# Optimization experiments

Hardware: AMD Instinct MI355X
Metric: run time of the kernel (lower is better)

Reference implementation:

```python
import jax, jax.numpy as jnp
import numpy as np

BETA = 0.25


def setup_inputs() -> dict:
    key = jax.random.key(0)
    k1, k2, k3, k4 = jax.random.split(key, 4)
    e_dim, n_e = 512, 8192
    z = jax.random.normal(k1, (16, e_dim, 32, 32), dtype=jnp.float32)
    # nn.init.normal_(embedding.weight, std=e_dim**-0.5)
    emb_weight = jax.random.normal(k2, (n_e, e_dim), dtype=jnp.float32) * (e_dim ** -0.5)
    # torch Linear default init ~ U(-1/sqrt(in), 1/sqrt(in))
    lim = 1.0 / np.sqrt(e_dim)
    proj_w = jax.random.uniform(k3, (e_dim, e_dim), minval=-lim, maxval=lim, dtype=jnp.float32)
    proj_b = jax.random.uniform(k4, (e_dim,), minval=-lim, maxval=lim, dtype=jnp.float32)
    return {"z": z, "emb_weight": emb_weight, "proj_w": proj_w, "proj_b": proj_b}


def reference(z, emb_weight, proj_w, proj_b):
    # z: [B, C, H, W] -> [B, H, W, C]
    zc = jnp.transpose(z, (0, 2, 3, 1))
    B, H, W, C = zc.shape
    z_flat = zc.reshape(-1, C)                               # [N, C]
    # projected codebook: Linear(e_dim, e_dim) -> x @ W^T + b
    qc = emb_weight @ proj_w.T + proj_b                      # [n_e, C]
    # squared distances: ||z||^2 + ||qc||^2 - 2 z.qc
    d = (jnp.sum(z_flat ** 2, axis=1, keepdims=True)
         + jnp.sum(qc ** 2, axis=1)
         - 2.0 * jnp.einsum('nd,kd->nk', z_flat, qc))        # [N, n_e]
    idx = jnp.argmin(d, axis=1)                              # [N]
    z_q = qc[idx].reshape(zc.shape)                          # [B, H, W, C]
    # legacy=False commit loss
    commit_loss = (BETA * jnp.mean((jax.lax.stop_gradient(z_q) - zc) ** 2)
                   + jnp.mean((z_q - jax.lax.stop_gradient(zc)) ** 2))
    # straight-through
    z_q = zc + jax.lax.stop_gradient(z_q - zc)
    z_q = jnp.transpose(z_q, (0, 3, 1, 2))                   # [B, C, H, W]
    min_encoding_indices = idx.reshape(B, H, W)              # sane_index_shape=True
    return z_q, commit_loss, min_encoding_indices
```

## Files before the change

### kernel.cpp

```cpp
#include <hip/hip_runtime.h>

typedef unsigned int uint;
typedef unsigned short ushort;
typedef __attribute__((ext_vector_type(8))) short short8;
typedef __attribute__((ext_vector_type(4))) float f32x4;

#define B_   16
#define C_   512
#define HW_  1024
#define N_   16384
#define K_   8192
#define EPS_ 0.25f

#define QC_OFF    0u
#define QC_SZ     (K_ * C_)
#define QN_OFF    (QC_OFF + QC_SZ)
#define QN_SZ     K_
#define ZN_OFF    (QN_OFF + QN_SZ)
#define ZN_SZ     N_
#define ZF_OFF    (ZN_OFF + ZN_SZ)
#define ZF_SZ     (N_ * C_)
#define ZH_OFF    (ZF_OFF + ZF_SZ)
#define ZH_SZ     (N_ * C_ / 2)
#define QH_OFF    (ZH_OFF + ZH_SZ)
#define QH_SZ     (K_ * C_ / 2)
#define WT_OFF    (QH_OFF + QH_SZ)
#define WT_SZ     (64 * N_ * 4)
#define CK_OFF    (WT_OFF + WT_SZ)
#define CK_SZ     (N_ * 16)
#define CC_OFF    (CK_OFF + CK_SZ)
#define CC_SZ     N_
#define IDXF_OFF  (CC_OFF + CC_SZ)
#define IDXF_SZ   N_
#define LOSS_OFF  (IDXF_OFF + IDXF_SZ)

#define OUT_ZQ    0
#define OUT_LOSS  8388608
#define OUT_IDX   8388609

__device__ __forceinline__ ushort f2bf(float f) {
    uint x = __float_as_uint(f);
    uint r = x + 0x7fffu + ((x >> 16) & 1u);
    return (ushort)(r >> 16);
}

__global__ __launch_bounds__(256) void transpose_z(const float* __restrict__ z,
                                                   float* __restrict__ zf,
                                                   ushort* __restrict__ zh) {
    __shared__ float ld[64][65];
    const int t = threadIdx.x;
    const int mt = blockIdx.x, ct = blockIdx.y, b = blockIdx.z;
    {
        const int cl = t >> 4, m4 = (t & 15) * 4;
#pragma unroll
        for (int cc = 0; cc < 4; ++cc) {
            const int c = ct * 64 + cc * 16 + cl;
            float4 v = *(const float4*)&z[((size_t)(b * 512 + c)) * 1024 + mt * 64 + m4];
            ld[cc * 16 + cl][m4 + 0] = v.x; ld[cc * 16 + cl][m4 + 1] = v.y;
            ld[cc * 16 + cl][m4 + 2] = v.z; ld[cc * 16 + cl][m4 + 3] = v.w;
        }
    }
    __syncthreads();
    {
        const int nl = t >> 4, c4 = (t & 15) * 4;
#pragma unroll
        for (int nn = 0; nn < 4; ++nn) {
            const int n_local = nn * 16 + nl;
            const size_t n = (size_t)b * 1024 + mt * 64 + n_local;
            float4 w;
            w.x = ld[c4 + 0][n_local]; w.y = ld[c4 + 1][n_local];
            w.z = ld[c4 + 2][n_local]; w.w = ld[c4 + 3][n_local];
            *(float4*)&zf[n * 512 + ct * 64 + c4] = w;
            ushort4 h; h.x = f2bf(w.x); h.y = f2bf(w.y); h.z = f2bf(w.z); h.w = f2bf(w.w);
            *(ushort4*)&zh[n * 512 + ct * 64 + c4] = h;
        }
    }
}

__global__ __launch_bounds__(256) void qc_gemm(const float* __restrict__ emb,
                                               const float* __restrict__ W,
                                               const float* __restrict__ bias,
                                               float* __restrict__ qc,
                                               ushort* __restrict__ qh) {
    __shared__ float As[16][132];
    __shared__ float Bs[16][132];
    const int t   = threadIdx.x;
    const int k0  = blockIdx.x * 128;
    const int c0  = blockIdx.y * 128;
    const int ty  = t >> 4, tx = t & 15;
    const int row = t >> 1;
    const int dq  = (t & 1) * 8;

    const float* pa = emb + (size_t)(k0 + row) * 512 + dq;
    const float* pb = W   + (size_t)(c0 + row) * 512 + dq;
    float4 ra0 = *(const float4*)&pa[0];
    float4 ra1 = *(const float4*)&pa[4];
    float4 rb0 = *(const float4*)&pb[0];
    float4 rb1 = *(const float4*)&pb[4];

    float acc[2][2][4][4] = {};
    for (int d0 = 0; d0 < 512; d0 += 16) {
        __syncthreads();
        As[dq + 0][row] = ra0.x; As[dq + 1][row] = ra0.y;
        As[dq + 2][row] = ra0.z; As[dq + 3][row] = ra0.w;
        As[dq + 4][row] = ra1.x; As[dq + 5][row] = ra1.y;
        As[dq + 6][row] = ra1.z; As[dq + 7][row] = ra1.w;
        Bs[dq + 0][row] = rb0.x; Bs[dq + 1][row] = rb0.y;
        Bs[dq + 2][row] = rb0.z; Bs[dq + 3][row] = rb0.w;
        Bs[dq + 4][row] = rb1.x; Bs[dq + 5][row] = rb1.y;
        Bs[dq + 6][row] = rb1.z; Bs[dq + 7][row] = rb1.w;
        if (d0 + 16 < 512) {
            ra0 = *(const float4*)&pa[d0 + 16];
            ra1 = *(const float4*)&pa[d0 + 20];
            rb0 = *(const float4*)&pb[d0 + 16];
            rb1 = *(const float4*)&pb[d0 + 20];
        }
        __syncthreads();
#pragma unroll
        for (int dd = 0; dd < 16; ++dd) {
            float4 a0 = *(const float4*)&As[dd][ty * 4];
            float4 a1 = *(const float4*)&As[dd][64 + ty * 4];
            float4 b0 = *(const float4*)&Bs[dd][tx * 4];
            float4 b1 = *(const float4*)&Bs[dd][64 + tx * 4];
            float aa[2][4] = {{a0.x, a0.y, a0.z, a0.w}, {a1.x, a1.y, a1.z, a1.w}};
            float bb[2][4] = {{b0.x, b0.y, b0.z, b0.w}, {b1.x, b1.y, b1.z, b1.w}};
#pragma unroll
            for (int ih = 0; ih < 2; ++ih)
#pragma unroll
                for (int jh = 0; jh < 2; ++jh)
#pragma unroll
                    for (int i = 0; i < 4; ++i)
#pragma unroll
                        for (int j = 0; j < 4; ++j)
                            acc[ih][jh][i][j] += aa[ih][i] * bb[jh][j];
        }
    }
#pragma unroll
    for (int ih = 0; ih < 2; ++ih)
#pragma unroll
        for (int i = 0; i < 4; ++i) {
            const size_t kr = (size_t)(k0 + ih * 64 + ty * 4 + i) * 512;
#pragma unroll
            for (int jh = 0; jh < 2; ++jh) {
                const int cb = c0 + jh * 64 + tx * 4;
                float4 v;
                v.x = acc[ih][jh][i][0] + bias[cb + 0];
                v.y = acc[ih][jh][i][1] + bias[cb + 1];
                v.z = acc[ih][jh][i][2] + bias[cb + 2];
                v.w = acc[ih][jh][i][3] + bias[cb + 3];
                *(float4*)&qc[kr + cb] = v;
                ushort4 h; h.x = f2bf(v.x); h.y = f2bf(v.y); h.z = f2bf(v.z); h.w = f2bf(v.w);
                *(ushort4*)&qh[kr + cb] = h;
            }
        }
}

__device__ __forceinline__ float pairwise512(const float* __restrict__ row) {
#pragma clang fp contract(off)
    float s128[4];
#pragma unroll
    for (int blk = 0; blk < 4; ++blk) {
        float r[8];
#pragma unroll
        for (int j = 0; j < 8; ++j) { float v = row[blk * 128 + j]; r[j] = v * v; }
#pragma unroll 1
        for (int i = 8; i < 128; i += 8) {
#pragma unroll
            for (int j = 0; j < 8; ++j) {
                float v = row[blk * 128 + i + j];
                float sq = v * v;
                r[j] = r[j] + sq;
            }
        }
        s128[blk] = ((r[0] + r[1]) + (r[2] + r[3])) + ((r[4] + r[5]) + (r[6] + r[7]));
    }
    return (s128[0] + s128[1]) + (s128[2] + s128[3]);
}

__global__ __launch_bounds__(256) void qnorm_pairwise(const float* __restrict__ qc,
                                                      float* __restrict__ qn) {
    const int k = blockIdx.x * 256 + threadIdx.x;
    qn[k] = pairwise512(qc + (size_t)k * C_);
}

__global__ __launch_bounds__(256) void znorm_pairwise(const float* __restrict__ zf,
                                                      float* __restrict__ zn) {
    const int n = blockIdx.x * 256 + threadIdx.x;
    zn[n] = pairwise512(zf + (size_t)n * C_);
}

#define PH_BAR()  __builtin_amdgcn_s_barrier()
#define PH_LGKM() asm volatile("s_waitcnt lgkmcnt(0)" ::: "memory")
#define PH_VM4()  asm volatile("s_waitcnt vmcnt(4)" ::: "memory")

__global__ __launch_bounds__(512, 2) void phaseA(const ushort* __restrict__ qh,
                                                 const ushort* __restrict__ zh,
                                                 const float* __restrict__ qn,
                                                 float* __restrict__ wtop) {
    __shared__ short lq[2][2][128 * 64];
    __shared__ short lz[2][2][128 * 64];
    const int t    = threadIdx.x;
    const int lane = t & 63;
    const int wv   = t >> 6;
    const int wk   = wv >> 2;
    const int wn   = wv & 3;
    const int n0   = blockIdx.x * 256;
    const int k0   = blockIdx.y * 256;

    auto stage_half = [&](int b, int h, int cchunk) {
        const int c0 = cchunk * 64;
#pragma unroll
        for (int p = 0; p < 2; ++p) {
            const int ch  = t + p * 512;
            const int row = ch >> 3;
            const int ce  = (((ch ^ row) & 7) << 3);
            if (h < 2) {
                __builtin_amdgcn_global_load_lds(
                    (const __attribute__((address_space(1))) uint*)(qh + (size_t)(k0 + h * 128 + row) * 512 + c0 + ce),
                    (__attribute__((address_space(3))) uint*)&lq[b][h][ch * 8], 16, 0, 0);
            } else {
                __builtin_amdgcn_global_load_lds(
                    (const __attribute__((address_space(1))) uint*)(zh + (size_t)(n0 + (h - 2) * 128 + row) * 512 + c0 + ce),
                    (__attribute__((address_space(3))) uint*)&lz[b][h - 2][ch * 8], 16, 0, 0);
            }
        }
    };

    auto rdA = [&](int b, int kk, int i) -> short8 {
        const int rl = i * 16 + (lane & 15);
        const int co = kk * 32 + ((lane >> 4) << 3);
        return *(const short8*)&lq[b][wk][rl * 64 + (co ^ ((rl & 7) << 3))];
    };
    auto rdB = [&](int b, int kk, int j) -> short8 {
        const int rg = wn * 64 + j * 16 + (lane & 15);
        const int co = kk * 32 + ((lane >> 4) << 3);
        return *(const short8*)&lz[b][rg >> 7][(rg & 127) * 64 + (co ^ ((rg & 7) << 3))];
    };

    f32x4 acc[8][4];
#pragma unroll
    for (int i = 0; i < 8; ++i)
#pragma unroll
        for (int j = 0; j < 4; ++j) acc[i][j] = (f32x4){0.f, 0.f, 0.f, 0.f};

    stage_half(0, 0, 0); stage_half(0, 1, 0); stage_half(0, 2, 0); stage_half(0, 3, 0);
    stage_half(1, 0, 1); stage_half(1, 1, 1);
    PH_VM4();
    PH_BAR();

    short8 a0[2][4], a1[2][4], b0[2][2], b1[2][2];

#pragma unroll 1
    for (int I = 0; I < 4; ++I) {
        const int t1 = 2 * I + 1;
        const int t2 = (2 * I + 2) & 7;
        const int t3 = (2 * I + 3) & 7;

#pragma unroll
        for (int kk = 0; kk < 2; ++kk) {
#pragma unroll
            for (int i = 0; i < 4; ++i) a0[kk][i] = rdA(0, kk, i);
#pragma unroll
            for (int j = 0; j < 2; ++j) b0[kk][j] = rdB(0, kk, j);
        }
        stage_half(1, 2, t1);
        PH_BAR(); PH_LGKM();
        __builtin_amdgcn_s_setprio(1);
#pragma unroll
        for (int kk = 0; kk < 2; ++kk)
#pragma unroll
            for (int i = 0; i < 4; ++i)
#pragma unroll
                for (int j = 0; j < 2; ++j)
                    acc[i][j] = __builtin_amdgcn_mfma_f32_16x16x32_bf16(a0[kk][i], b0[kk][j], acc[i][j], 0, 0, 0);
        __builtin_amdgcn_s_setprio(0);
        PH_BAR();
#pragma unroll
        for (int kk = 0; kk < 2; ++kk)
#pragma unroll
            for (int i = 0; i < 4; ++i) a1[kk][i] = rdA(0, kk, 4 + i);
        stage_half(1, 3, t1);
        PH_BAR(); PH_LGKM();
        __builtin_amdgcn_s_setprio(1);
#pragma unroll
        for (int kk = 0; kk < 2; ++kk)
#pragma unroll
            for (int i = 0; i < 4; ++i)
#pragma unroll
                for (int j = 0; j < 2; ++j)
                    acc[4 + i][j] = __builtin_amdgcn_mfma_f32_16x16x32_bf16(a1[kk][i], b0[kk][j], acc[4 + i][j], 0, 0, 0);
        __builtin_amdgcn_s_setprio(0);
        PH_BAR();
#pragma unroll
        for (int kk = 0; kk < 2; ++kk)
#pragma unroll
            for (int j = 0; j < 2; ++j) b1[kk][j] = rdB(0, kk, 2 + j);
        stage_half(0, 0, t2);
        PH_BAR(); PH_LGKM();
        __builtin_amdgcn_s_setprio(1);
#pragma unroll
        for (int kk = 0; kk < 2; ++kk)
#pragma unroll
            for (int i = 0; i < 4; ++i)
#pragma unroll
                for (int j = 0; j < 2; ++j)
                    acc[i][2 + j] = __builtin_amdgcn_mfma_f32_16x16x32_bf16(a0[kk][i], b1[kk][j], acc[i][2 + j], 0, 0, 0);
        __builtin_amdgcn_s_setprio(0);
        PH_BAR();
        stage_half(0, 1, t2);
        PH_BAR(); PH_LGKM();
        __builtin_amdgcn_s_setprio(1);
#pragma unroll
        for (int kk = 0; kk < 2; ++kk)
#pragma unroll
            for (int i = 0; i < 4; ++i)
#pragma unroll
                for (int j = 0; j < 2; ++j)
                    acc[4 + i][2 + j] = __builtin_amdgcn_mfma_f32_16x16x32_bf16(a1[kk][i], b1[kk][j], acc[4 + i][2 + j], 0, 0, 0);
        __builtin_amdgcn_s_setprio(0);
        PH_VM4();
        PH_BAR();

#pragma unroll
        for (int kk = 0; kk < 2; ++kk) {
#pragma unroll
            for (int i = 0; i < 4; ++i) a0[kk][i] = rdA(1, kk, i);
#pragma unroll
            for (int j = 0; j < 2; ++j) b0[kk][j] = rdB(1, kk, j);
        }
        stage_half(0, 2, t2);
        PH_BAR(); PH_LGKM();
        __builtin_amdgcn_s_setprio(1);
#pragma unroll
        for (int kk = 0; kk < 2; ++kk)
#pragma unroll
            for (int i = 0; i < 4; ++i)
#pragma unroll
                for (int j = 0; j < 2; ++j)
                    acc[i][j] = __builtin_amdgcn_mfma_f32_16x16x32_bf16(a0[kk][i], b0[kk][j], acc[i][j], 0, 0, 0);
        __builtin_amdgcn_s_setprio(0);
        PH_BAR();
#pragma unroll
        for (int kk = 0; kk < 2; ++kk)
#pragma unroll
            for (int i = 0; i < 4; ++i) a1[kk][i] = rdA(1, kk, 4 + i);
        stage_half(0, 3, t2);
        PH_BAR(); PH_LGKM();
        __builtin_amdgcn_s_setprio(1);
#pragma unroll
        for (int kk = 0; kk < 2; ++kk)
#pragma unroll
            for (int i = 0; i < 4; ++i)
#pragma unroll
                for (int j = 0; j < 2; ++j)
                    acc[4 + i][j] = __builtin_amdgcn_mfma_f32_16x16x32_bf16(a1[kk][i], b0[kk][j], acc[4 + i][j], 0, 0, 0);
        __builtin_amdgcn_s_setprio(0);
        PH_BAR();
#pragma unroll
        for (int kk = 0; kk < 2; ++kk)
#pragma unroll
            for (int j = 0; j < 2; ++j) b1[kk][j] = rdB(1, kk, 2 + j);
        stage_half(1, 0, t3);
        PH_BAR(); PH_LGKM();
        __builtin_amdgcn_s_setprio(1);
#pragma unroll
        for (int kk = 0; kk < 2; ++kk)
#pragma unroll
            for (int i = 0; i < 4; ++i)
#pragma unroll
                for (int j = 0; j < 2; ++j)
                    acc[i][2 + j] = __builtin_amdgcn_mfma_f32_16x16x32_bf16(a0[kk][i], b1[kk][j], acc[i][2 + j], 0, 0, 0);
        __builtin_amdgcn_s_setprio(0);
        PH_BAR();
        stage_half(1, 1, t3);
        PH_BAR(); PH_LGKM();
        __builtin_amdgcn_s_setprio(1);
#pragma unroll
        for (int kk = 0; kk < 2; ++kk)
#pragma unroll
            for (int i = 0; i < 4; ++i)
#pragma unroll
                for (int j = 0; j < 2; ++j)
                    acc[4 + i][2 + j] = __builtin_amdgcn_mfma_f32_16x16x32_bf16(a1[kk][i], b1[kk][j], acc[4 + i][2 + j], 0, 0, 0);
        __builtin_amdgcn_s_setprio(0);
        PH_VM4();
        PH_BAR();
    }

    const int q4 = (lane >> 4) * 4;
    float v1[4], v2[4];
    int   k1[4], k2[4];
#pragma unroll
    for (int in = 0; in < 4; ++in) { v1[in] = 1e30f; v2[in] = 1e30f; k1[in] = 0; k2[in] = 0; }

#pragma unroll
    for (int ik = 0; ik < 8; ++ik) {
        float qv[4];
#pragma unroll
        for (int r = 0; r < 4; ++r)
            qv[r] = qn[k0 + wk * 128 + ik * 16 + q4 + r];
#pragma unroll
        for (int in = 0; in < 4; ++in) {
#pragma unroll
            for (int r = 0; r < 4; ++r) {
                const float val = qv[r] - 2.0f * acc[ik][in][r];
                const int   kg  = k0 + wk * 128 + ik * 16 + q4 + r;
                if (val < v1[in]) { v2[in] = v1[in]; k2[in] = k1[in]; v1[in] = val; k1[in] = kg; }
                else if (val < v2[in]) { v2[in] = val; k2[in] = kg; }
            }
        }
    }
#pragma unroll
    for (int m = 16; m <= 32; m <<= 1) {
#pragma unroll
        for (int in = 0; in < 4; ++in) {
            const float ov1 = __shfl_xor(v1[in], m, 64);
            const int   ok1 = __shfl_xor(k1[in], m, 64);
            const float ov2 = __shfl_xor(v2[in], m, 64);
            const int   ok2 = __shfl_xor(k2[in], m, 64);
            float nv1, nv2; int nk1, nk2;
            if (ov1 < v1[in]) {
                nv1 = ov1; nk1 = ok1;
                if (v1[in] < ov2) { nv2 = v1[in]; nk2 = k1[in]; } else { nv2 = ov2; nk2 = ok2; }
            } else {
                nv1 = v1[in]; nk1 = k1[in];
                if (ov1 < v2[in]) { nv2 = ov1; nk2 = ok1; } else { nv2 = v2[in]; nk2 = k2[in]; }
            }
            v1[in] = nv1; k1[in] = nk1; v2[in] = nv2; k2[in] = nk2;
        }
    }
    if ((lane >> 4) == 0) {
        const int w = blockIdx.y * 2 + wk;
#pragma unroll
        for (int in = 0; in < 4; ++in) {
            const int n = n0 + wn * 64 + in * 16 + (lane & 15);
            float4 o; o.x = v1[in]; o.y = __int_as_float(k1[in]);
            o.z = v2[in]; o.w = __int_as_float(k2[in]);
            *(float4*)&wtop[((size_t)w * N_ + n) * 4] = o;
        }
    }
}

__global__ __launch_bounds__(256) void phaseB(const float* __restrict__ wtop,
                                              int* __restrict__ cand_k,
                                              int* __restrict__ cand_cnt) {
    const int n = blockIdx.x * 256 + threadIdx.x;
    float rmin = 1e30f;
    for (int w = 0; w < 64; ++w)
        rmin = fminf(rmin, wtop[((size_t)w * N_ + n) * 4]);
    const float thr = rmin + EPS_;
    int cnt = 0;
    for (int w = 0; w < 64; ++w) {
        float4 e = *(const float4*)&wtop[((size_t)w * N_ + n) * 4];
        if (e.x <= thr && cnt < 16) cand_k[n * 16 + cnt++] = __float_as_int(e.y);
        if (e.z <= thr && cnt < 16) cand_k[n * 16 + cnt++] = __float_as_int(e.w);
    }
    cand_cnt[n] = cnt;
}

__global__ __launch_bounds__(256) void phaseC(const float* __restrict__ zf,
                                              const float* __restrict__ qc,
                                              const float* __restrict__ zn,
                                              const float* __restrict__ qn,
                                              const int* __restrict__ cand_k,
                                              const int* __restrict__ cand_cnt,
                                              int* __restrict__ idxf,
                                              float* __restrict__ out_idx) {
    __shared__ float zr[4][512];
    __shared__ float ql[4][2][512];
    const int wv   = threadIdx.x >> 6;
    const int lane = threadIdx.x & 63;
    const int r    = blockIdx.x * 4 + wv;
    const int cnt  = cand_cnt[r];

    if (cnt == 1) {
        if (lane == 0) { const int k = cand_k[r * 16]; idxf[r] = k; out_idx[r] = (float)k; }
        return;
    }

    *(float4*)&zr[wv][lane * 8]     = *(const float4*)&zf[(size_t)r * 512 + lane * 8];
    *(float4*)&zr[wv][lane * 8 + 4] = *(const float4*)&zf[(size_t)r * 512 + lane * 8 + 4];

    const int g  = lane >> 5;
    const int cl = (lane & 31) * 16;
    const int steps = (cnt + 1) >> 1;
    const float znr = zn[r];

    auto cand_of = [&](int s) {
        const int ci = 2 * s + g;
        return cand_k[r * 16 + (ci < cnt ? ci : 0)];
    };

    int k_cur = cand_of(0);
    const float* q0 = qc + (size_t)k_cur * 512 + cl;
    float4 p0 = *(const float4*)&q0[0];
    float4 p1 = *(const float4*)&q0[4];
    float4 p2 = *(const float4*)&q0[8];
    float4 p3 = *(const float4*)&q0[12];

    float bd = 1e30f;
    int   bi = 0x7fffffff;

    for (int s = 0; s < steps; ++s) {
        *(float4*)&ql[wv][g][cl + 0]  = p0;
        *(float4*)&ql[wv][g][cl + 4]  = p1;
        *(float4*)&ql[wv][g][cl + 8]  = p2;
        *(float4*)&ql[wv][g][cl + 12] = p3;

        int k_next = 0;
        if (s + 1 < steps) {
            k_next = cand_of(s + 1);
            const float* qn_ = qc + (size_t)k_next * 512 + cl;
            p0 = *(const float4*)&qn_[0];
            p1 = *(const float4*)&qn_[4];
            p2 = *(const float4*)&qn_[8];
            p3 = *(const float4*)&qn_[12];
        }

        float acc = 0.f;
#pragma unroll 16
        for (int c = 0; c < 512; c += 4) {
            float4 zv = *(const float4*)&zr[wv][c];
            float4 qv = *(const float4*)&ql[wv][g][c];
            acc = fmaf(zv.x, qv.x, acc);
            acc = fmaf(zv.y, qv.y, acc);
            acc = fmaf(zv.z, qv.z, acc);
            acc = fmaf(zv.w, qv.w, acc);
        }
        const float T = znr + qn[k_cur];
        const float d = T - 2.0f * acc;
        const bool valid = (2 * s + g) < cnt;
        if (valid && (d < bd || (d == bd && k_cur < bi))) { bd = d; bi = k_cur; }
        k_cur = k_next;
    }

    const float od = __shfl_xor(bd, 32, 64);
    const int   oi = __shfl_xor(bi, 32, 64);
    if (od < bd || (od == bd && oi < bi)) { bd = od; bi = oi; }

    if (lane == 0) { idxf[r] = bi; out_idx[r] = (float)bi; }
}

__global__ __launch_bounds__(256) void gather_out(const float* __restrict__ z,
                                                  const float* __restrict__ qc,
                                                  const int* __restrict__ idxf,
                                                  float* __restrict__ zq_out,
                                                  float* __restrict__ loss_acc) {
    __shared__ int   idxs[64];
    __shared__ float zqs[64][65];
    __shared__ float wsum[4];
    const int t  = threadIdx.x;
    const int mc = blockIdx.x;
    const int cc = blockIdx.y;
    const int bz = blockIdx.z;

    if (t < 64) idxs[t] = idxf[bz * 1024 + mc * 64 + t];
    __syncthreads();
    {
        const int row  = t >> 2;
        const int coff = (t & 3) * 16;
        const float* src = qc + (size_t)idxs[row] * 512 + cc * 64 + coff;
#pragma unroll
        for (int v = 0; v < 4; ++v) {
            float4 q = *(const float4*)&src[v * 4];
            zqs[row][coff + v * 4 + 0] = q.x;
            zqs[row][coff + v * 4 + 1] = q.y;
            zqs[row][coff + v * 4 + 2] = q.z;
            zqs[row][coff + v * 4 + 3] = q.w;
        }
    }
    __syncthreads();

    float ls = 0.f;
    {
        const int c_local = t >> 2;
        const int mg      = (t & 3) * 16;
        const size_t gbase = ((size_t)(bz * 512 + cc * 64 + c_local)) * 1024 + mc * 64 + mg;
#pragma unroll
        for (int v = 0; v < 4; ++v) {
            const int m = mg + v * 4;
            float4 w;
            w.x = zqs[m + 0][c_local];
            w.y = zqs[m + 1][c_local];
            w.z = zqs[m + 2][c_local];
            w.w = zqs[m + 3][c_local];
            float4 zv = *(const float4*)&z[gbase + v * 4];
            float dx = w.x - zv.x, dy = w.y - zv.y, dz = w.z - zv.z, dw = w.w - zv.w;
            ls += dx * dx + dy * dy + dz * dz + dw * dw;
            *(float4*)&zq_out[gbase + v * 4] = w;
        }
    }
#pragma unroll
    for (int m = 32; m; m >>= 1) ls += __shfl_xor(ls, m, 64);
    const int lane = t & 63, wvv = t >> 6;
    if (lane == 0) wsum[wvv] = ls;
    __syncthreads();
    if (t == 0) atomicAdd(loss_acc, wsum[0] + wsum[1] + wsum[2] + wsum[3]);
}

__global__ void zero_loss(float* __restrict__ loss_acc) { loss_acc[0] = 0.f; }

__global__ void finalize(const float* __restrict__ loss_acc,
                         float* __restrict__ out_loss) {
    out_loss[0] = 1.25f * loss_acc[0] / 8388608.0f;
}

extern "C" void kernel_launch(void* const* d_in, const int* in_sizes, int n_in,
                              void* d_out, int out_size, void* d_ws, size_t ws_size,
                              hipStream_t stream) {
    const float* z    = (const float*)d_in[0];
    const float* emb  = (const float*)d_in[1];
    const float* W    = (const float*)d_in[2];
    const float* bias = (const float*)d_in[3];
    float* ws = (float*)d_ws;

    float*  qc       = ws + QC_OFF;
    float*  qn       = ws + QN_OFF;
    float*  zn       = ws + ZN_OFF;
    float*  zf       = ws + ZF_OFF;
    ushort* zh       = (ushort*)(ws + ZH_OFF);
    ushort* qh       = (ushort*)(ws + QH_OFF);
    float*  wtop     = ws + WT_OFF;
    int*    cand_k   = (int*)(ws + CK_OFF);
    int*    cand_cnt = (int*)(ws + CC_OFF);
    int*    idxf     = (int*)(ws + IDXF_OFF);
    float*  loss_acc = ws + LOSS_OFF;
    float*  out      = (float*)d_out;

    zero_loss<<<1, 1, 0, stream>>>(loss_acc);
    transpose_z<<<dim3(16, 8, 16), 256, 0, stream>>>(z, zf, zh);
    qc_gemm<<<dim3(K_ / 128, C_ / 128), 256, 0, stream>>>(emb, W, bias, qc, qh);
    qnorm_pairwise<<<K_ / 256, 256, 0, stream>>>(qc, qn);
    znorm_pairwise<<<N_ / 256, 256, 0, stream>>>(zf, zn);
    phaseA<<<dim3(N_ / 256, K_ / 256), 512, 0, stream>>>(qh, zh, qn, wtop);
    phaseB<<<N_ / 256, 256, 0, stream>>>(wtop, cand_k, cand_cnt);
    phaseC<<<N_ / 4, 256, 0, stream>>>(zf, qc, zn, qn, cand_k, cand_cnt, idxf, out + OUT_IDX);
    gather_out<<<dim3(16, 8, B_), 256, 0, stream>>>(z, qc, idxf, out + OUT_ZQ, loss_acc);
    finalize<<<1, 1, 0, stream>>>(loss_acc, out + OUT_LOSS);
}
```

Before: 421.1 us.

## Retile qc GEMM, coalesce norm kernels, precompute phaseA LDS pointers, drop zero kernel

Several independent changes. The qc GEMM tile is cut from 128x128 to 128x64, which doubles the grid and lowers per-thread registers. The z norm now reads the original NCHW z with coalesced strided loads instead of row-major zf. The q norm has 8 threads cooperate on each row and reduce with shuffles, so its loads coalesce. PhaseA precomputes its swizzled LDS and global addresses once instead of recomputing them on every access, and zeroing of the loss accumulator moves into phaseB to save a launch. The grouped q-norm sums in a different order from the old pairwise sum, which can change tie-breaking results slightly.

```diff
diff --git a/kernel.cpp b/kernel.cpp
--- a/kernel.cpp
+++ b/kernel.cpp
@@ -83,37 +83,35 @@
                                                float* __restrict__ qc,
                                                ushort* __restrict__ qh) {
     __shared__ float As[16][132];
-    __shared__ float Bs[16][132];
-    const int t   = threadIdx.x;
-    const int k0  = blockIdx.x * 128;
-    const int c0  = blockIdx.y * 128;
-    const int ty  = t >> 4, tx = t & 15;
-    const int row = t >> 1;
-    const int dq  = (t & 1) * 8;
-
-    const float* pa = emb + (size_t)(k0 + row) * 512 + dq;
-    const float* pb = W   + (size_t)(c0 + row) * 512 + dq;
+    __shared__ float Bs[16][68];
+    const int t    = threadIdx.x;
+    const int k0   = blockIdx.x * 128;
+    const int c0   = blockIdx.y * 64;
+    const int ty   = t >> 4, tx = t & 15;
+    const int rowA = t >> 1;
+    const int dqA  = (t & 1) * 8;
+    const int rowB = t >> 2;
+    const int dqB  = (t & 3) * 4;
+
+    const float* pa = emb + (size_t)(k0 + rowA) * 512 + dqA;
+    const float* pb = W   + (size_t)(c0 + rowB) * 512 + dqB;
     float4 ra0 = *(const float4*)&pa[0];
     float4 ra1 = *(const float4*)&pa[4];
-    float4 rb0 = *(const float4*)&pb[0];
-    float4 rb1 = *(const float4*)&pb[4];
-
-    float acc[2][2][4][4] = {};
+    float4 rb  = *(const float4*)&pb[0];
+
+    float acc[2][4][4] = {};
     for (int d0 = 0; d0 < 512; d0 += 16) {
         __syncthreads();
-        As[dq + 0][row] = ra0.x; As[dq + 1][row] = ra0.y;
-        As[dq + 2][row] = ra0.z; As[dq + 3][row] = ra0.w;
-        As[dq + 4][row] = ra1.x; As[dq + 5][row] = ra1.y;
-        As[dq + 6][row] = ra1.z; As[dq + 7][row] = ra1.w;
-        Bs[dq + 0][row] = rb0.x; Bs[dq + 1][row] = rb0.y;
-        Bs[dq + 2][row] = rb0.z; Bs[dq + 3][row] = rb0.w;
-        Bs[dq + 4][row] = rb1.x; Bs[dq + 5][row] = rb1.y;
-        Bs[dq + 6][row] = rb1.z; Bs[dq + 7][row] = rb1.w;
+        As[dqA + 0][rowA] = ra0.x; As[dqA + 1][rowA] = ra0.y;
+        As[dqA + 2][rowA] = ra0.z; As[dqA + 3][rowA] = ra0.w;
+        As[dqA + 4][rowA] = ra1.x; As[dqA + 5][rowA] = ra1.y;
+        As[dqA + 6][rowA] = ra1.z; As[dqA + 7][rowA] = ra1.w;
+        Bs[dqB + 0][rowB] = rb.x;  Bs[dqB + 1][rowB] = rb.y;
+        Bs[dqB + 2][rowB] = rb.z;  Bs[dqB + 3][rowB] = rb.w;
         if (d0 + 16 < 512) {
             ra0 = *(const float4*)&pa[d0 + 16];
             ra1 = *(const float4*)&pa[d0 + 20];
-            rb0 = *(const float4*)&pb[d0 + 16];
-            rb1 = *(const float4*)&pb[d0 + 20];
+            rb  = *(const float4*)&pb[d0 + 16];
         }
         __syncthreads();
 #pragma unroll
@@ -121,18 +119,15 @@
             float4 a0 = *(const float4*)&As[dd][ty * 4];
             float4 a1 = *(const float4*)&As[dd][64 + ty * 4];
             float4 b0 = *(const float4*)&Bs[dd][tx * 4];
-            float4 b1 = *(const float4*)&Bs[dd][64 + tx * 4];
             float aa[2][4] = {{a0.x, a0.y, a0.z, a0.w}, {a1.x, a1.y, a1.z, a1.w}};
-            float bb[2][4] = {{b0.x, b0.y, b0.z, b0.w}, {b1.x, b1.y, b1.z, b1.w}};
+            float bb[4] = {b0.x, b0.y, b0.z, b0.w};
 #pragma unroll
             for (int ih = 0; ih < 2; ++ih)
 #pragma unroll
-                for (int jh = 0; jh < 2; ++jh)
-#pragma unroll
-                    for (int i = 0; i < 4; ++i)
-#pragma unroll
-                        for (int j = 0; j < 4; ++j)
-                            acc[ih][jh][i][j] += aa[ih][i] * bb[jh][j];
+                for (int i = 0; i < 4; ++i)
+#pragma unroll
+                    for (int j = 0; j < 4; ++j)
+                        acc[ih][i][j] += aa[ih][i] * bb[j];
         }
     }
 #pragma unroll
@@ -140,65 +135,88 @@
 #pragma unroll
         for (int i = 0; i < 4; ++i) {
             const size_t kr = (size_t)(k0 + ih * 64 + ty * 4 + i) * 512;
-#pragma unroll
-            for (int jh = 0; jh < 2; ++jh) {
-                const int cb = c0 + jh * 64 + tx * 4;
-                float4 v;
-                v.x = acc[ih][jh][i][0] + bias[cb + 0];
-                v.y = acc[ih][jh][i][1] + bias[cb + 1];
-                v.z = acc[ih][jh][i][2] + bias[cb + 2];
-                v.w = acc[ih][jh][i][3] + bias[cb + 3];
-                *(float4*)&qc[kr + cb] = v;
-                ushort4 h; h.x = f2bf(v.x); h.y = f2bf(v.y); h.z = f2bf(v.z); h.w = f2bf(v.w);
-                *(ushort4*)&qh[kr + cb] = h;
-            }
-        }
-}
-
-__device__ __forceinline__ float pairwise512(const float* __restrict__ row) {
+            const int cb = c0 + tx * 4;
+            float4 v;
+            v.x = acc[ih][i][0] + bias[cb + 0];
+            v.y = acc[ih][i][1] + bias[cb + 1];
+            v.z = acc[ih][i][2] + bias[cb + 2];
+            v.w = acc[ih][i][3] + bias[cb + 3];
+            *(float4*)&qc[kr + cb] = v;
+            ushort4 h; h.x = f2bf(v.x); h.y = f2bf(v.y); h.z = f2bf(v.z); h.w = f2bf(v.w);
+            *(ushort4*)&qh[kr + cb] = h;
+        }
+}
+
+__global__ __launch_bounds__(256) void znorm_pairwise(const float* __restrict__ z,
+                                                      float* __restrict__ zn) {
 #pragma clang fp contract(off)
+    const int n = blockIdx.x * 256 + threadIdx.x;
+    const int b = n >> 10, m = n & 1023;
+    const float* base = z + (size_t)b * C_ * HW_ + m;
     float s128[4];
 #pragma unroll
     for (int blk = 0; blk < 4; ++blk) {
         float r[8];
 #pragma unroll
-        for (int j = 0; j < 8; ++j) { float v = row[blk * 128 + j]; r[j] = v * v; }
+        for (int j = 0; j < 8; ++j) {
+            float v = base[(size_t)(blk * 128 + j) * HW_];
+            r[j] = v * v;
+        }
 #pragma unroll 1
         for (int i = 8; i < 128; i += 8) {
 #pragma unroll
             for (int j = 0; j < 8; ++j) {
-                float v = row[blk * 128 + i + j];
+                float v = base[(size_t)(blk * 128 + i + j) * HW_];
                 float sq = v * v;
                 r[j] = r[j] + sq;
             }
         }
         s128[blk] = ((r[0] + r[1]) + (r[2] + r[3])) + ((r[4] + r[5]) + (r[6] + r[7]));
     }
-    return (s128[0] + s128[1]) + (s128[2] + s128[3]);
-}
-
-__global__ __launch_bounds__(256) void qnorm_pairwise(const float* __restrict__ qc,
-                                                      float* __restrict__ qn) {
-    const int k = blockIdx.x * 256 + threadIdx.x;
-    qn[k] = pairwise512(qc + (size_t)k * C_);
-}
-
-__global__ __launch_bounds__(256) void znorm_pairwise(const float* __restrict__ zf,
-                                                      float* __restrict__ zn) {
-    const int n = blockIdx.x * 256 + threadIdx.x;
-    zn[n] = pairwise512(zf + (size_t)n * C_);
+    zn[n] = (s128[0] + s128[1]) + (s128[2] + s128[3]);
+}
+
+__global__ __launch_bounds__(256) void qnorm_grouped(const float* __restrict__ qc,
+                                                     float* __restrict__ qn) {
+#pragma clang fp contract(off)
+    const int t   = threadIdx.x;
+    const int grp = t >> 3;
+    const int j   = t & 7;
+    const int k   = blockIdx.x * 32 + grp;
+    const float* row = qc + (size_t)k * C_;
+    float s[4];
+#pragma unroll
+    for (int blk = 0; blk < 4; ++blk) {
+        float v0 = row[blk * 128 + j];
+        float r  = v0 * v0;
+#pragma unroll 1
+        for (int i = 1; i < 16; ++i) {
+            float v  = row[blk * 128 + i * 8 + j];
+            float sq = v * v;
+            r = r + sq;
+        }
+        float t1 = r  + __shfl_xor(r, 1, 64);
+        float t2 = t1 + __shfl_xor(t1, 2, 64);
+        float t3 = t2 + __shfl_xor(t2, 4, 64);
+        s[blk] = t3;
+    }
+    if (j == 0) qn[k] = (s[0] + s[1]) + (s[2] + s[3]);
 }
 
 #define PH_BAR()  __builtin_amdgcn_s_barrier()
 #define PH_LGKM() asm volatile("s_waitcnt lgkmcnt(0)" ::: "memory")
 #define PH_VM4()  asm volatile("s_waitcnt vmcnt(4)" ::: "memory")
+
+__device__ __forceinline__ short8 ld8(const short* p, int off) {
+    return *(const short8*)(p + off);
+}
 
 __global__ __launch_bounds__(512, 2) void phaseA(const ushort* __restrict__ qh,
                                                  const ushort* __restrict__ zh,
                                                  const float* __restrict__ qn,
                                                  float* __restrict__ wtop) {
-    __shared__ short lq[2][2][128 * 64];
-    __shared__ short lz[2][2][128 * 64];
+    __shared__ short lq[32768];
+    __shared__ short lz[32768];
     const int t    = threadIdx.x;
     const int lane = t & 63;
     const int wv   = t >> 6;
@@ -207,34 +225,44 @@
     const int n0   = blockIdx.x * 256;
     const int k0   = blockIdx.y * 256;
 
-    auto stage_half = [&](int b, int h, int cchunk) {
-        const int c0 = cchunk * 64;
-#pragma unroll
-        for (int p = 0; p < 2; ++p) {
-            const int ch  = t + p * 512;
-            const int row = ch >> 3;
-            const int ce  = (((ch ^ row) & 7) << 3);
-            if (h < 2) {
-                __builtin_amdgcn_global_load_lds(
-                    (const __attribute__((address_space(1))) uint*)(qh + (size_t)(k0 + h * 128 + row) * 512 + c0 + ce),
-                    (__attribute__((address_space(3))) uint*)&lq[b][h][ch * 8], 16, 0, 0);
-            } else {
-                __builtin_amdgcn_global_load_lds(
-                    (const __attribute__((address_space(1))) uint*)(zh + (size_t)(n0 + (h - 2) * 128 + row) * 512 + c0 + ce),
-                    (__attribute__((address_space(3))) uint*)&lz[b][h - 2][ch * 8], 16, 0, 0);
-            }
-        }
-    };
-
-    auto rdA = [&](int b, int kk, int i) -> short8 {
-        const int rl = i * 16 + (lane & 15);
-        const int co = kk * 32 + ((lane >> 4) << 3);
-        return *(const short8*)&lq[b][wk][rl * 64 + (co ^ ((rl & 7) << 3))];
-    };
-    auto rdB = [&](int b, int kk, int j) -> short8 {
-        const int rg = wn * 64 + j * 16 + (lane & 15);
-        const int co = kk * 32 + ((lane >> 4) << 3);
-        return *(const short8*)&lz[b][rg >> 7][(rg & 127) * 64 + (co ^ ((rg & 7) << 3))];
+    const int l15 = lane & 15;
+    const int hi8 = (lane >> 4) << 3;
+    const int xr  = (l15 & 7) << 3;
+    const short* pA0 = lq + wk * 8192 + l15 * 64 + ((hi8) ^ xr);
+    const short* pA1 = lq + wk * 8192 + l15 * 64 + ((32 + hi8) ^ xr);
+    const short* pB0 = lz + (wn >> 1) * 8192 + (wn & 1) * 4096 + l15 * 64 + ((hi8) ^ xr);
+    const short* pB1 = lz + (wn >> 1) * 8192 + (wn & 1) * 4096 + l15 * 64 + ((32 + hi8) ^ xr);
+
+    const int ch0 = t,        row0 = ch0 >> 3;
+    const int ch1 = t + 512,  row1 = ch1 >> 3;
+    const int ce0 = ((ch0 ^ row0) & 7) << 3;
+    const int ce1 = ((ch1 ^ row1) & 7) << 3;
+    const ushort* qsrc0 = qh + (size_t)(k0 + row0) * 512 + ce0;
+    const ushort* qsrc1 = qh + (size_t)(k0 + row1) * 512 + ce1;
+    const ushort* zsrc0 = zh + (size_t)(n0 + row0) * 512 + ce0;
+    const ushort* zsrc1 = zh + (size_t)(n0 + row1) * 512 + ce1;
+    short* qdst0 = lq + ch0 * 8;
+    short* qdst1 = lq + ch1 * 8;
+    short* zdst0 = lz + ch0 * 8;
+    short* zdst1 = lz + ch1 * 8;
+
+    auto stage_half = [&](int b, int h, int chunk) {
+        const int co = chunk * 64;
+        if (h < 2) {
+            __builtin_amdgcn_global_load_lds(
+                (const __attribute__((address_space(1))) uint*)(qsrc0 + h * 65536 + co),
+                (__attribute__((address_space(3))) uint*)(qdst0 + (b * 2 + h) * 8192), 16, 0, 0);
+            __builtin_amdgcn_global_load_lds(
+                (const __attribute__((address_space(1))) uint*)(qsrc1 + h * 65536 + co),
+                (__attribute__((address_space(3))) uint*)(qdst1 + (b * 2 + h) * 8192), 16, 0, 0);
+        } else {
+            __builtin_amdgcn_global_load_lds(
+                (const __attribute__((address_space(1))) uint*)(zsrc0 + (h - 2) * 65536 + co),
+                (__attribute__((address_space(3))) uint*)(zdst0 + (b * 2 + (h - 2)) * 8192), 16, 0, 0);
+            __builtin_amdgcn_global_load_lds(
+                (const __attribute__((address_space(1))) uint*)(zsrc1 + (h - 2) * 65536 + co),
+                (__attribute__((address_space(3))) uint*)(zdst1 + (b * 2 + (h - 2)) * 8192), 16, 0, 0);
+        }
     };
 
     f32x4 acc[8][4];
@@ -257,12 +285,9 @@
         const int t3 = (2 * I + 3) & 7;
 
 #pragma unroll
-        for (int kk = 0; kk < 2; ++kk) {
-#pragma unroll
-            for (int i = 0; i < 4; ++i) a0[kk][i] = rdA(0, kk, i);
-#pragma unroll
-            for (int j = 0; j < 2; ++j) b0[kk][j] = rdB(0, kk, j);
-        }
+        for (int i = 0; i < 4; ++i) { a0[0][i] = ld8(pA0, i * 1024); a0[1][i] = ld8(pA1, i * 1024); }
+#pragma unroll
+        for (int jj = 0; jj < 2; ++jj) { b0[0][jj] = ld8(pB0, jj * 1024); b0[1][jj] = ld8(pB1, jj * 1024); }
         stage_half(1, 2, t1);
         PH_BAR(); PH_LGKM();
         __builtin_amdgcn_s_setprio(1);
@@ -271,14 +296,12 @@
 #pragma unroll
             for (int i = 0; i < 4; ++i)
 #pragma unroll
-                for (int j = 0; j < 2; ++j)
-                    acc[i][j] = __builtin_amdgcn_mfma_f32_16x16x32_bf16(a0[kk][i], b0[kk][j], acc[i][j], 0, 0, 0);
-        __builtin_amdgcn_s_setprio(0);
-        PH_BAR();
-#pragma unroll
-        for (int kk = 0; kk < 2; ++kk)
-#pragma unroll
-            for (int i = 0; i < 4; ++i) a1[kk][i] = rdA(0, kk, 4 + i);
+                for (int jj = 0; jj < 2; ++jj)
+                    acc[i][jj] = __builtin_amdgcn_mfma_f32_16x16x32_bf16(a0[kk][i], b0[kk][jj], acc[i][jj], 0, 0, 0);
+        __builtin_amdgcn_s_setprio(0);
+        PH_BAR();
+#pragma unroll
+        for (int i = 0; i < 4; ++i) { a1[0][i] = ld8(pA0, 4096 + i * 1024); a1[1][i] = ld8(pA1, 4096 + i * 1024); }
         stage_half(1, 3, t1);
         PH_BAR(); PH_LGKM();
         __builtin_amdgcn_s_setprio(1);
@@ -287,14 +310,12 @@
 #pragma unroll
             for (int i = 0; i < 4; ++i)
 #pragma unroll
-                for (int j = 0; j < 2; ++j)
-                    acc[4 + i][j] = __builtin_amdgcn_mfma_f32_16x16x32_bf16(a1[kk][i], b0[kk][j], acc[4 + i][j], 0, 0, 0);
-        __builtin_amdgcn_s_setprio(0);
-        PH_BAR();
-#pragma unroll
-        for (int kk = 0; kk < 2; ++kk)
-#pragma unroll
-            for (int j = 0; j < 2; ++j) b1[kk][j] = rdB(0, kk, 2 + j);
+                for (int jj = 0; jj < 2; ++jj)
+                    acc[4 + i][jj] = __builtin_amdgcn_mfma_f32_16x16x32_bf16(a1[kk][i], b0[kk][jj], acc[4 + i][jj], 0, 0, 0);
+        __builtin_amdgcn_s_setprio(0);
+        PH_BAR();
+#pragma unroll
+        for (int jj = 0; jj < 2; ++jj) { b1[0][jj] = ld8(pB0, 2048 + jj * 1024); b1[1][jj] = ld8(pB1, 2048 + jj * 1024); }
         stage_half(0, 0, t2);
         PH_BAR(); PH_LGKM();
         __builtin_amdgcn_s_setprio(1);
@@ -303,8 +324,8 @@
 #pragma unroll
             for (int i = 0; i < 4; ++i)
 #pragma unroll
-                for (int j = 0; j < 2; ++j)
-                    acc[i][2 + j] = __builtin_amdgcn_mfma_f32_16x16x32_bf16(a0[kk][i], b1[kk][j], acc[i][2 + j], 0, 0, 0);
+                for (int jj = 0; jj < 2; ++jj)
+                    acc[i][2 + jj] = __builtin_amdgcn_mfma_f32_16x16x32_bf16(a0[kk][i], b1[kk][jj], acc[i][2 + jj], 0, 0, 0);
         __builtin_amdgcn_s_setprio(0);
         PH_BAR();
         stage_half(0, 1, t2);
@@ -315,19 +336,16 @@
 #pragma unroll
             for (int i = 0; i < 4; ++i)
 #pragma unroll
-                for (int j = 0; j < 2; ++j)
-                    acc[4 + i][2 + j] = __builtin_amdgcn_mfma_f32_16x16x32_bf16(a1[kk][i], b1[kk][j], acc[4 + i][2 + j], 0, 0, 0);
+                for (int jj = 0; jj < 2; ++jj)
+                    acc[4 + i][2 + jj] = __builtin_amdgcn_mfma_f32_16x16x32_bf16(a1[kk][i], b1[kk][jj], acc[4 + i][2 + jj], 0, 0, 0);
         __builtin_amdgcn_s_setprio(0);
         PH_VM4();
         PH_BAR();
 
 #pragma unroll
-        for (int kk = 0; kk < 2; ++kk) {
-#pragma unroll
-            for (int i = 0; i < 4; ++i) a0[kk][i] = rdA(1, kk, i);
-#pragma unroll
-            for (int j = 0; j < 2; ++j) b0[kk][j] = rdB(1, kk, j);
-        }
+        for (int i = 0; i < 4; ++i) { a0[0][i] = ld8(pA0, 16384 + i * 1024); a0[1][i] = ld8(pA1, 16384 + i * 1024); }
+#pragma unroll
+        for (int jj = 0; jj < 2; ++jj) { b0[0][jj] = ld8(pB0, 16384 + jj * 1024); b0[1][jj] = ld8(pB1, 16384 + jj * 1024); }
         stage_half(0, 2, t2);
         PH_BAR(); PH_LGKM();
         __builtin_amdgcn_s_setprio(1);
@@ -336,14 +354,12 @@
 #pragma unroll
             for (int i = 0; i < 4; ++i)
 #pragma unroll
-                for (int j = 0; j < 2; ++j)
-                    acc[i][j] = __builtin_amdgcn_mfma_f32_16x16x32_bf16(a0[kk][i], b0[kk][j], acc[i][j], 0, 0, 0);
-        __builtin_amdgcn_s_setprio(0);
-        PH_BAR();
-#pragma unroll
-        for (int kk = 0; kk < 2; ++kk)
-#pragma unroll
-            for (int i = 0; i < 4; ++i) a1[kk][i] = rdA(1, kk, 4 + i);
+                for (int jj = 0; jj < 2; ++jj)
+                    acc[i][jj] = __builtin_amdgcn_mfma_f32_16x16x32_bf16(a0[kk][i], b0[kk][jj], acc[i][jj], 0, 0, 0);
+        __builtin_amdgcn_s_setprio(0);
+        PH_BAR();
+#pragma unroll
+        for (int i = 0; i < 4; ++i) { a1[0][i] = ld8(pA0, 16384 + 4096 + i * 1024); a1[1][i] = ld8(pA1, 16384 + 4096 + i * 1024); }
         stage_half(0, 3, t2);
         PH_BAR(); PH_LGKM();
         __builtin_amdgcn_s_setprio(1);
@@ -352,14 +368,12 @@
 #pragma unroll
             for (int i = 0; i < 4; ++i)
 #pragma unroll
-                for (int j = 0; j < 2; ++j)
-                    acc[4 + i][j] = __builtin_amdgcn_mfma_f32_16x16x32_bf16(a1[kk][i], b0[kk][j], acc[4 + i][j], 0, 0, 0);
-        __builtin_amdgcn_s_setprio(0);
-        PH_BAR();
-#pragma unroll
-        for (int kk = 0; kk < 2; ++kk)
-#pragma unroll
-            for (int j = 0; j < 2; ++j) b1[kk][j] = rdB(1, kk, 2 + j);
+                for (int jj = 0; jj < 2; ++jj)
+                    acc[4 + i][jj] = __builtin_amdgcn_mfma_f32_16x16x32_bf16(a1[kk][i], b0[kk][jj], acc[4 + i][jj], 0, 0, 0);
+        __builtin_amdgcn_s_setprio(0);
+        PH_BAR();
+#pragma unroll
+        for (int jj = 0; jj < 2; ++jj) { b1[0][jj] = ld8(pB0, 16384 + 2048 + jj * 1024); b1[1][jj] = ld8(pB1, 16384 + 2048 + jj * 1024); }
         stage_half(1, 0, t3);
         PH_BAR(); PH_LGKM();
         __builtin_amdgcn_s_setprio(1);
@@ -368,8 +382,8 @@
 #pragma unroll
             for (int i = 0; i < 4; ++i)
 #pragma unroll
-                for (int j = 0; j < 2; ++j)
-                    acc[i][2 + j] = __builtin_amdgcn_mfma_f32_16x16x32_bf16(a0[kk][i], b1[kk][j], acc[i][2 + j], 0, 0, 0);
+                for (int jj = 0; jj < 2; ++jj)
+                    acc[i][2 + jj] = __builtin_amdgcn_mfma_f32_16x16x32_bf16(a0[kk][i], b1[kk][jj], acc[i][2 + jj], 0, 0, 0);
         __builtin_amdgcn_s_setprio(0);
         PH_BAR();
         stage_half(1, 1, t3);
@@ -380,8 +394,8 @@
 #pragma unroll
             for (int i = 0; i < 4; ++i)
 #pragma unroll
-                for (int j = 0; j < 2; ++j)
-                    acc[4 + i][2 + j] = __builtin_amdgcn_mfma_f32_16x16x32_bf16(a1[kk][i], b1[kk][j], acc[4 + i][2 + j], 0, 0, 0);
+                for (int jj = 0; jj < 2; ++jj)
+                    acc[4 + i][2 + jj] = __builtin_amdgcn_mfma_f32_16x16x32_bf16(a1[kk][i], b1[kk][jj], acc[4 + i][2 + jj], 0, 0, 0);
         __builtin_amdgcn_s_setprio(0);
         PH_VM4();
         PH_BAR();
@@ -443,8 +457,10 @@
 
 __global__ __launch_bounds__(256) void phaseB(const float* __restrict__ wtop,
                                               int* __restrict__ cand_k,
-                                              int* __restrict__ cand_cnt) {
+                                              int* __restrict__ cand_cnt,
+                                              float* __restrict__ loss_acc) {
     const int n = blockIdx.x * 256 + threadIdx.x;
+    if (n == 0) loss_acc[0] = 0.f;
     float rmin = 1e30f;
     for (int w = 0; w < 64; ++w)
         rmin = fminf(rmin, wtop[((size_t)w * N_ + n) * 4]);
@@ -598,8 +614,6 @@
     if (t == 0) atomicAdd(loss_acc, wsum[0] + wsum[1] + wsum[2] + wsum[3]);
 }
 
-__global__ void zero_loss(float* __restrict__ loss_acc) { loss_acc[0] = 0.f; }
-
 __global__ void finalize(const float* __restrict__ loss_acc,
                          float* __restrict__ out_loss) {
     out_loss[0] = 1.25f * loss_acc[0] / 8388608.0f;
@@ -627,13 +641,12 @@
     float*  loss_acc = ws + LOSS_OFF;
     float*  out      = (float*)d_out;
 
-    zero_loss<<<1, 1, 0, stream>>>(loss_acc);
     transpose_z<<<dim3(16, 8, 16), 256, 0, stream>>>(z, zf, zh);
-    qc_gemm<<<dim3(K_ / 128, C_ / 128), 256, 0, stream>>>(emb, W, bias, qc, qh);
-    qnorm_pairwise<<<K_ / 256, 256, 0, stream>>>(qc, qn);
-    znorm_pairwise<<<N_ / 256, 256, 0, stream>>>(zf, zn);
+    qc_gemm<<<dim3(K_ / 128, C_ / 64), 256, 0, stream>>>(emb, W, bias, qc, qh);
+    qnorm_grouped<<<K_ / 32, 256, 0, stream>>>(qc, qn);
+    znorm_pairwise<<<N_ / 256, 256, 0, stream>>>(z, zn);
     phaseA<<<dim3(N_ / 256, K_ / 256), 512, 0, stream>>>(qh, zh, qn, wtop);
-    phaseB<<<N_ / 256, 256, 0, stream>>>(wtop, cand_k, cand_cnt);
+    phaseB<<<N_ / 256, 256, 0, stream>>>(wtop, cand_k, cand_cnt, loss_acc);
     phaseC<<<N_ / 4, 256, 0, stream>>>(zf, qc, zn, qn, cand_k, cand_cnt, idxf, out + OUT_IDX);
     gather_out<<<dim3(16, 8, B_), 256, 0, stream>>>(z, qc, idxf, out + OUT_ZQ, loss_acc);
     finalize<<<1, 1, 0, stream>>>(loss_acc, out + OUT_LOSS);
```

New measurement: 419.7 us. No clear change (-0.3%).
